# Kernel tuning notes

Measured on AMD Instinct MI355X. Metric: run time of the kernel, lower is better.

## Reference

```python
import jax, jax.numpy as jnp
import numpy as np

B, S, D_IN, D_OUT, H = 2, 2048, 1024, 1024, 16
HD = D_OUT // H  # 64


def setup_inputs() -> dict:
    key = jax.random.key(0)
    ks = jax.random.split(key, 6)
    s = 0.02
    return {
        "x": jax.random.normal(ks[0], (B, S, D_IN), dtype=jnp.float32),
        "W_q": jax.random.normal(ks[1], (D_IN, D_OUT), dtype=jnp.float32) * s,
        "W_k": jax.random.normal(ks[2], (D_IN, D_OUT), dtype=jnp.float32) * s,
        "W_v": jax.random.normal(ks[3], (D_IN, D_OUT), dtype=jnp.float32) * s,
        "W_o": jax.random.normal(ks[4], (D_OUT, D_OUT), dtype=jnp.float32) * s,
        "b_o": jax.random.normal(ks[5], (D_OUT,), dtype=jnp.float32) * s,
    }


def reference(x, W_q, W_k, W_v, W_o, b_o):
    b, n, _ = x.shape
    # project and split heads: [b, h, n, hd]
    q = (x @ W_q).reshape(b, n, H, HD).transpose(0, 2, 1, 3)
    k = (x @ W_k).reshape(b, n, H, HD).transpose(0, 2, 1, 3)
    v = (x @ W_v).reshape(b, n, H, HD).transpose(0, 2, 1, 3)
    scores = jnp.einsum("bhqd,bhkd->bhqk", q, k) / jnp.sqrt(jnp.float32(HD))
    causal = jnp.tril(jnp.ones((n, n), dtype=bool))
    scores = jnp.where(causal, scores, -jnp.inf)
    attn = jax.nn.softmax(scores, axis=-1)  # dropout p=0.0 -> identity
    ctx = jnp.einsum("bhqk,bhkd->bhqd", attn, v)
    ctx = ctx.transpose(0, 2, 1, 3).reshape(b, n, D_OUT)
    return ctx @ W_o + b_o
```

## Files before the change

kernel.cpp:

```cpp
#include <hip/hip_runtime.h>

#define B_    2
#define S_    2048
#define DIN   1024
#define DOUT  1024
#define H_    16
#define HD_   64
#define M_    (B_ * S_)

typedef __bf16 bf16x8 __attribute__((ext_vector_type(8)));
typedef float  f32x4  __attribute__((ext_vector_type(4)));

__device__ __forceinline__ f32x4 MFMA(bf16x8 a, bf16x8 b, f32x4 c) {
    return __builtin_amdgcn_mfma_f32_16x16x32_bf16(a, b, c, 0, 0, 0);
}

__device__ __forceinline__ unsigned short f2b(float f) {
    union { float f; unsigned int u; } v; v.f = f;
    unsigned int u = v.u;
    return (unsigned short)((u + 0x7fffu + ((u >> 16) & 1u)) >> 16);
}

__device__ __forceinline__ unsigned pack2(float a, float b) {
    union { __bf16 h[2]; unsigned u; } cv;
    cv.h[0] = (__bf16)a; cv.h[1] = (__bf16)b;
    return cv.u;
}

#define GLDS(gp, lp) __builtin_amdgcn_global_load_lds( \
    (const __attribute__((address_space(1))) void*)(gp), \
    (__attribute__((address_space(3))) void*)(lp), 16, 0, 0)

#define QSCALE 0.1803368801111204f

__global__ __launch_bounds__(256) void k_cvt_all(const float* __restrict__ x,
                                                 const float* __restrict__ Wq,
                                                 const float* __restrict__ Wk,
                                                 const float* __restrict__ Wv,
                                                 const float* __restrict__ Wo,
                                                 unsigned short* __restrict__ xb,
                                                 unsigned short* __restrict__ WqkvT,
                                                 unsigned short* __restrict__ WoT) {
    __shared__ __align__(16) float tile[64][68];
    int bid = blockIdx.x;
    int tid = threadIdx.x;
    if (bid < 1024) {
#pragma unroll
        for (int j = 0; j < 4; j++) {
            int i = bid * 4096 + j * 1024 + tid * 4;
            float4 v = *reinterpret_cast<const float4*>(x + i);
            ushort4 o;
            o.x = f2b(v.x); o.y = f2b(v.y); o.z = f2b(v.z); o.w = f2b(v.w);
            *reinterpret_cast<ushort4*>(xb + i) = o;
        }
        return;
    }
    int wb = bid - 1024;
    int w = wb >> 8;
    int t = wb & 255;
    const float* src = (w == 0) ? Wq : (w == 1) ? Wk : (w == 2) ? Wv : Wo;
    unsigned short* dst = (w < 3) ? WqkvT + (size_t)w * 1024 * DIN : WoT;
    int k0 = (t >> 4) * 64, n0 = (t & 15) * 64;
#pragma unroll
    for (int j = 0; j < 4; j++) {
        int idx = j * 256 + tid;
        int r = idx >> 4, c4g = idx & 15;
        int sg = c4g ^ ((r >> 3) & 7);
        *reinterpret_cast<float4*>(&tile[r][sg * 4]) =
            *reinterpret_cast<const float4*>(&src[(size_t)(k0 + r) * DOUT + n0 + c4g * 4]);
    }
    __syncthreads();
#pragma unroll
    for (int j = 0; j < 2; j++) {
        int idx = j * 256 + tid;
        int n = idx >> 3, gk = (idx & 7) * 8;
        int g = n >> 2, e = n & 3;
        unsigned short o[8];
#pragma unroll
        for (int u = 0; u < 8; u++) {
            int k = gk + u;
            o[u] = f2b(tile[k][((g ^ ((k >> 3) & 7)) << 2) + e]);
        }
        *reinterpret_cast<int4*>(&dst[(size_t)(n0 + n) * DIN + k0 + gk]) =
            *reinterpret_cast<int4*>(o);
    }
}

template <int OUT_MODE, int BM>
__global__ __launch_bounds__(256) void k_gemm(const unsigned short* __restrict__ A,
                                              const unsigned short* __restrict__ Bt,
                                              unsigned short* __restrict__ Cq,
                                              unsigned short* __restrict__ Ck,
                                              unsigned short* __restrict__ Cvt,
                                              float* __restrict__ Cf,
                                              const float* __restrict__ bias,
                                              int M, int N, int K, int bxg) {
    constexpr int MI  = BM / 32;
    constexpr int ASZ = BM * 32;
    constexpr int BSZ = 128 * 32;
    constexpr int ACH = BM / 64;
    constexpr int STG = 2 * (ASZ + BSZ);
    constexpr int SMEM_N = (OUT_MODE == 0 && STG < 17408) ? 17408 : STG;
    __shared__ __align__(16) unsigned short smem[SMEM_N];

    int bid = blockIdx.x;
    int xcd = bid & 7;
    int r = bid >> 3;
    int byg = (M / BM) >> 2;
    int by = (xcd >> 1) * byg + r / bxg;
    int bx = (xcd & 1) * bxg + r % bxg;
    int m0 = by * BM, n0 = bx * 128;

    int tid = threadIdx.x;
    int wid = tid >> 6, lane = tid & 63;
    int wm = wid >> 1, wn = wid & 1;
    int lr = lane & 15, lg = lane >> 4;

    f32x4 acc[MI][4] = {};

    int srow = lane >> 2;
    int scol = ((lane & 3) ^ (srow & 3)) * 8;
    int runit = (lg ^ (lr & 3)) * 8;

#define STAGE_G(buf, k0)                                                       \
    {                                                                          \
        unsigned short* Ad = smem + (buf) * ASZ;                               \
        unsigned short* Bd = smem + 2 * ASZ + (buf) * BSZ;                     \
        _Pragma("unroll")                                                      \
        for (int c = 0; c < ACH; c++) {                                        \
            int chunk = wid * ACH + c;                                         \
            int row = chunk * 16 + srow;                                       \
            GLDS(A + (size_t)(m0 + row) * K + (k0) + scol,                     \
                 (char*)Ad + chunk * 1024);                                    \
        }                                                                      \
        _Pragma("unroll")                                                      \
        for (int c = 0; c < 2; c++) {                                          \
            int chunk = wid * 2 + c;                                           \
            int row = chunk * 16 + srow;                                       \
            GLDS(Bt + (size_t)(n0 + row) * K + (k0) + scol,                    \
                 (char*)Bd + chunk * 1024);                                    \
        }                                                                      \
    }

    STAGE_G(0, 0)
    __syncthreads();

    int nkt = K >> 5;
    for (int kt = 0; kt < nkt; kt++) {
        int buf = kt & 1;
        if (kt + 1 < nkt) STAGE_G(buf ^ 1, (kt + 1) * 32)

        const unsigned short* Asr = smem + buf * ASZ;
        const unsigned short* Bsr = smem + 2 * ASZ + buf * BSZ;
        bf16x8 af[MI], bf[4];
#pragma unroll
        for (int mi = 0; mi < MI; mi++)
            af[mi] = *reinterpret_cast<const bf16x8*>(
                &Asr[(wm * (BM / 2) + mi * 16 + lr) * 32 + runit]);
#pragma unroll
        for (int ni = 0; ni < 4; ni++)
            bf[ni] = *reinterpret_cast<const bf16x8*>(
                &Bsr[(wn * 64 + ni * 16 + lr) * 32 + runit]);
#pragma unroll
        for (int mi = 0; mi < MI; mi++)
#pragma unroll
            for (int ni = 0; ni < 4; ni++)
                acc[mi][ni] = MFMA(af[mi], bf[ni], acc[mi][ni]);

        asm volatile("s_waitcnt vmcnt(0)" ::: "memory");
        __builtin_amdgcn_s_barrier();
    }

    if (OUT_MODE == 2) {
        for (int mi = 0; mi < MI; mi++)
            for (int ni = 0; ni < 4; ni++)
                for (int i = 0; i < 4; i++) {
                    int row = m0 + wm * (BM / 2) + mi * 16 + lg * 4 + i;
                    int col = n0 + wn * 64 + ni * 16 + lr;
                    Cf[(size_t)row * N + col] = acc[mi][ni][i] + bias[col];
                }
    } else if (n0 < 2048) {
        unsigned short* Cd = (n0 < 1024) ? Cq : Ck;
        int cb = (n0 < 1024) ? 0 : 1024;
        float sc = (n0 < 1024) ? QSCALE : 1.0f;
        for (int mi = 0; mi < MI; mi++)
            for (int ni = 0; ni < 4; ni++)
                for (int i = 0; i < 4; i++) {
                    int row = m0 + wm * (BM / 2) + mi * 16 + lg * 4 + i;
                    int col = n0 + wn * 64 + ni * 16 + lr;
                    Cd[(size_t)row * 1024 + (col - cb)] = f2b(acc[mi][ni][i] * sc);
                }
    } else {
        unsigned short* Lt = smem;
        for (int mi = 0; mi < MI; mi++)
            for (int ni = 0; ni < 4; ni++) {
                int cl = wn * 64 + ni * 16 + lr;
                int rl0 = wm * (BM / 2) + mi * 16 + lg * 4;
                uint2 wd;
                wd.x = pack2(acc[mi][ni][0], acc[mi][ni][1]);
                wd.y = pack2(acc[mi][ni][2], acc[mi][ni][3]);
                *reinterpret_cast<uint2*>(&Lt[cl * 136 + rl0]) = wd;
            }
        __syncthreads();
        int b = m0 >> 11, ms = m0 & (S_ - 1);
        int bh64 = (b * H_ + ((n0 - 2048) >> 6)) * 64;
#pragma unroll
        for (int it = 0; it < 4; it++) {
            int cl = it * 32 + (tid >> 3);
            int ss = (tid & 7) * 16;
            int4 v0 = *reinterpret_cast<int4*>(&Lt[cl * 136 + ss]);
            int4 v1 = *reinterpret_cast<int4*>(&Lt[cl * 136 + ss + 8]);
            unsigned short* dp = Cvt + (size_t)(bh64 + cl) * S_ + ms + ss;
            *reinterpret_cast<int4*>(dp) = v0;
            *reinterpret_cast<int4*>(dp + 8) = v1;
        }
    }
#undef STAGE_G
}

__global__ __launch_bounds__(512, 4) void k_attn(const unsigned short* __restrict__ Q,
                                                 const unsigned short* __restrict__ Kg,
                                                 const unsigned short* __restrict__ Vt,
                                                 unsigned short* __restrict__ ctx) {
    int bid = blockIdx.x;
    int xcd = bid & 7;
    int k   = bid >> 3;
    int p   = k >> 2;
    int bh  = xcd * 4 + (k & 3);
    int b = bh >> 4, h = bh & 15;
    int tid = threadIdx.x, wid = tid >> 6, lane = tid & 63;
    int lr = lane & 15, lg = lane >> 4;
    int qtB = 31 - p;
    int qt = (wid < 4) ? qtB : p;
    int q0 = qt * 64 + (wid & 3) * 16;

    __shared__ __align__(16) unsigned short Ks[4][64 * 64];
    __shared__ __align__(16) unsigned short Vs[4][64 * 64];
    __shared__ __align__(16) unsigned p_lds32[8][16 * 32];
    unsigned* pl32 = p_lds32[wid];

    const unsigned short* Qp = Q  + (size_t)b * S_ * DOUT + (size_t)h * HD_;
    const unsigned short* Kp = Kg + (size_t)b * S_ * DOUT + (size_t)h * HD_;
    const unsigned short* Vp = Vt + (size_t)(b * H_ + h) * HD_ * S_;

    bf16x8 qf0 = *reinterpret_cast<const bf16x8*>(&Qp[(size_t)(q0 + lr) * DOUT + lg * 8]);
    bf16x8 qf1 = *reinterpret_cast<const bf16x8*>(&Qp[(size_t)(q0 + lr) * DOUT + 32 + lg * 8]);
    asm volatile("" : "+v"(qf0), "+v"(qf1));

    int srow = lane >> 3;
    int scol = ((lane & 7) ^ srow) * 8;

#define STAGE_KV(buf, t)                                                           \
    {                                                                              \
        int kv0_ = (t) * 64;                                                       \
        int krow = wid * 8 + srow;                                                 \
        GLDS(Kp + (size_t)(kv0_ + krow) * DOUT + scol,                             \
             (char*)&Ks[buf][0] + wid * 1024);                                     \
        GLDS(Vp + (size_t)krow * S_ + kv0_ + scol,                                 \
             (char*)&Vs[buf][0] + wid * 1024);                                     \
    }

    int ntile = qtB + 1;
    STAGE_KV(0, 0)
    STAGE_KV(1, 1)

    f32x4 o[4] = {};
    float l = 0.f;
    int rxor = (lr & 7) << 4;
    int qg = q0 + lr;

    int cur = 0;
    for (int t = 0; t < ntile; t++) {
        int ahead = ntile - 1 - t;
        if (ahead >= 2) {
            STAGE_KV((cur + 2) & 3, t + 2)
            asm volatile("s_waitcnt vmcnt(4)" ::: "memory");
        } else if (ahead == 1) {
            asm volatile("s_waitcnt vmcnt(2)" ::: "memory");
        } else {
            asm volatile("s_waitcnt vmcnt(0)" ::: "memory");
        }
        __builtin_amdgcn_s_barrier();

        if (t <= qt) {
            const unsigned short* Kt = Ks[cur];
            const unsigned short* Vl = Vs[cur];
            int kv0 = t * 64;

            f32x4 s[4] = {};
            __builtin_amdgcn_s_setprio(1);
#pragma unroll
            for (int nf = 0; nf < 4; nf++)
#pragma unroll
                for (int kk = 0; kk < 2; kk++) {
                    bf16x8 kf = *reinterpret_cast<const bf16x8*>(
                        &Kt[(nf * 16 + lr) * 64 + (((kk * 64 + lg * 16) ^ rxor) >> 1)]);
                    s[nf] = MFMA(kf, kk ? qf1 : qf0, s[nf]);
                }
            __builtin_amdgcn_s_setprio(0);

            if (t == qt) {
#pragma unroll
                for (int nf = 0; nf < 4; nf++)
#pragma unroll
                    for (int i = 0; i < 4; i++)
                        if (kv0 + nf * 16 + lg * 4 + i > qg) s[nf][i] = -2000.0f;
            }

            f32x4 acc = {};
#pragma unroll
            for (int nf = 0; nf < 4; nf++) {
                f32x4 pv;
#pragma unroll
                for (int i = 0; i < 4; i++) pv[i] = exp2f(s[nf][i]);
                acc += pv;
                int unit = (nf * 2 + (lg >> 1)) ^ (lr & 7);
                uint2 wd; wd.x = pack2(pv[0], pv[1]); wd.y = pack2(pv[2], pv[3]);
                *reinterpret_cast<uint2*>(&pl32[lr * 32 + unit * 4 + (lg & 1) * 2]) = wd;
            }
            l += (acc[0] + acc[1]) + (acc[2] + acc[3]);

            bf16x8 pf[2];
#pragma unroll
            for (int kvb = 0; kvb < 2; kvb++)
                pf[kvb] = *reinterpret_cast<const bf16x8*>(
                    &pl32[lr * 32 + (((kvb * 4 + lg) ^ (lr & 7)) * 4)]);

            __builtin_amdgcn_s_setprio(1);
#pragma unroll
            for (int nd = 0; nd < 4; nd++)
#pragma unroll
                for (int kk = 0; kk < 2; kk++) {
                    bf16x8 vf = *reinterpret_cast<const bf16x8*>(
                        &Vl[(nd * 16 + lr) * 64 + (((kk * 64 + lg * 16) ^ rxor) >> 1)]);
                    o[nd] = MFMA(pf[kk], vf, o[nd]);
                }
            __builtin_amdgcn_s_setprio(0);
        }

        cur = (cur + 1) & 3;
    }

    l += __shfl_xor(l, 16, 64);
    l += __shfl_xor(l, 32, 64);

#pragma unroll
    for (int i = 0; i < 4; i++) {
        float li = __shfl(l, lg * 4 + i, 16);
        float r = __builtin_amdgcn_rcpf(li);
#pragma unroll
        for (int nd = 0; nd < 4; nd++)
            ((__bf16*)ctx)[((size_t)b * S_ + q0 + lg * 4 + i) * DOUT + h * HD_ + nd * 16 + lr] =
                (__bf16)(o[nd][i] * r);
    }
#undef STAGE_KV
}

extern "C" void kernel_launch(void* const* d_in, const int* in_sizes, int n_in,
                              void* d_out, int out_size, void* d_ws, size_t ws_size,
                              hipStream_t stream) {
    const float* x  = (const float*)d_in[0];
    const float* Wq = (const float*)d_in[1];
    const float* Wk = (const float*)d_in[2];
    const float* Wv = (const float*)d_in[3];
    const float* Wo = (const float*)d_in[4];
    const float* bo = (const float*)d_in[5];
    float* out = (float*)d_out;
    char* ws = (char*)d_ws;
    const size_t MB = 1u << 20;

    unsigned short* xb    = (unsigned short*)(ws);
    unsigned short* ctx   = (unsigned short*)(ws);
    unsigned short* WqkvT = (unsigned short*)(ws + 8 * MB);
    unsigned short* WoT   = (unsigned short*)(ws + 14 * MB);
    unsigned short* Qb    = (unsigned short*)(ws + 16 * MB);
    unsigned short* Kb    = (unsigned short*)(ws + 24 * MB);
    unsigned short* Vtb   = (unsigned short*)(ws + 32 * MB);

    (void)in_sizes; (void)n_in; (void)out_size; (void)ws_size;

    k_cvt_all<<<2048, 256, 0, stream>>>(x, Wq, Wk, Wv, Wo, xb, WqkvT, WoT);

    k_gemm<0, 128><<<768, 256, 0, stream>>>(xb, WqkvT, Qb, Kb, Vtb, nullptr, nullptr,
                                            M_, 3072, DIN, 12);

    k_attn<<<512, 512, 0, stream>>>(Qb, Kb, Vtb, ctx);

    k_gemm<2, 64><<<512, 256, 0, stream>>>(ctx, WoT, nullptr, nullptr, nullptr,
                                           out, bo, M_, DOUT, DOUT, 4);
}
```

Baseline: 101.0 us.

## Replace double-buffered K32 GEMM pipeline with single-buffer K64 tiles

The projection GEMM now stages 64-wide K tiles into a single shared buffer, using an 8-way XOR swizzle, instead of double-buffering 32-wide tiles. Each tile does two MFMA k-steps between two __syncthreads per iteration. This halves the number of loop iterations and barriers per K and keeps shared memory usage the same, but global loads no longer overlap with MFMA compute, so load latency is exposed every iteration.

```diff
diff --git a/kernel.cpp b/kernel.cpp
--- a/kernel.cpp
+++ b/kernel.cpp
@@ -96,12 +96,14 @@
                                               const float* __restrict__ bias,
                                               int M, int N, int K, int bxg) {
     constexpr int MI  = BM / 32;
-    constexpr int ASZ = BM * 32;
-    constexpr int BSZ = 128 * 32;
-    constexpr int ACH = BM / 64;
-    constexpr int STG = 2 * (ASZ + BSZ);
+    constexpr int ASZ = BM * 64;
+    constexpr int BSZ = 128 * 64;
+    constexpr int ACH = BM / 32;
+    constexpr int STG = ASZ + BSZ;
     constexpr int SMEM_N = (OUT_MODE == 0 && STG < 17408) ? 17408 : STG;
     __shared__ __align__(16) unsigned short smem[SMEM_N];
+    unsigned short* As = smem;
+    unsigned short* Bs = smem + ASZ;
 
     int bid = blockIdx.x;
     int xcd = bid & 7;
@@ -118,57 +120,43 @@
 
     f32x4 acc[MI][4] = {};
 
-    int srow = lane >> 2;
-    int scol = ((lane & 3) ^ (srow & 3)) * 8;
-    int runit = (lg ^ (lr & 3)) * 8;
-
-#define STAGE_G(buf, k0)                                                       \
-    {                                                                          \
-        unsigned short* Ad = smem + (buf) * ASZ;                               \
-        unsigned short* Bd = smem + 2 * ASZ + (buf) * BSZ;                     \
-        _Pragma("unroll")                                                      \
-        for (int c = 0; c < ACH; c++) {                                        \
-            int chunk = wid * ACH + c;                                         \
-            int row = chunk * 16 + srow;                                       \
-            GLDS(A + (size_t)(m0 + row) * K + (k0) + scol,                     \
-                 (char*)Ad + chunk * 1024);                                    \
-        }                                                                      \
-        _Pragma("unroll")                                                      \
-        for (int c = 0; c < 2; c++) {                                          \
-            int chunk = wid * 2 + c;                                           \
-            int row = chunk * 16 + srow;                                       \
-            GLDS(Bt + (size_t)(n0 + row) * K + (k0) + scol,                    \
-                 (char*)Bd + chunk * 1024);                                    \
-        }                                                                      \
-    }
-
-    STAGE_G(0, 0)
-    __syncthreads();
-
-    int nkt = K >> 5;
-    for (int kt = 0; kt < nkt; kt++) {
-        int buf = kt & 1;
-        if (kt + 1 < nkt) STAGE_G(buf ^ 1, (kt + 1) * 32)
-
-        const unsigned short* Asr = smem + buf * ASZ;
-        const unsigned short* Bsr = smem + 2 * ASZ + buf * BSZ;
-        bf16x8 af[MI], bf[4];
-#pragma unroll
-        for (int mi = 0; mi < MI; mi++)
-            af[mi] = *reinterpret_cast<const bf16x8*>(
-                &Asr[(wm * (BM / 2) + mi * 16 + lr) * 32 + runit]);
-#pragma unroll
-        for (int ni = 0; ni < 4; ni++)
-            bf[ni] = *reinterpret_cast<const bf16x8*>(
-                &Bsr[(wn * 64 + ni * 16 + lr) * 32 + runit]);
-#pragma unroll
-        for (int mi = 0; mi < MI; mi++)
+    int srow = lane >> 3;
+    int scol = ((lane & 7) ^ srow) * 8;
+    int rsw  = lr & 7;
+
+    for (int k0 = 0; k0 < K; k0 += 64) {
+#pragma unroll
+        for (int c = 0; c < ACH; c++) {
+            int chunk = wid * ACH + c;
+            int row = chunk * 8 + srow;
+            GLDS(A + (size_t)(m0 + row) * K + k0 + scol, (char*)As + chunk * 1024);
+        }
+#pragma unroll
+        for (int c = 0; c < 4; c++) {
+            int chunk = wid * 4 + c;
+            int row = chunk * 8 + srow;
+            GLDS(Bt + (size_t)(n0 + row) * K + k0 + scol, (char*)Bs + chunk * 1024);
+        }
+        __syncthreads();
+
+#pragma unroll
+        for (int kk = 0; kk < 2; kk++) {
+            bf16x8 af[MI], bf[4];
+#pragma unroll
+            for (int mi = 0; mi < MI; mi++)
+                af[mi] = *reinterpret_cast<const bf16x8*>(
+                    &As[(wm * (BM / 2) + mi * 16 + lr) * 64 + (((kk * 4 + lg) ^ rsw) * 8)]);
 #pragma unroll
             for (int ni = 0; ni < 4; ni++)
-                acc[mi][ni] = MFMA(af[mi], bf[ni], acc[mi][ni]);
-
-        asm volatile("s_waitcnt vmcnt(0)" ::: "memory");
-        __builtin_amdgcn_s_barrier();
+                bf[ni] = *reinterpret_cast<const bf16x8*>(
+                    &Bs[(wn * 64 + ni * 16 + lr) * 64 + (((kk * 4 + lg) ^ rsw) * 8)]);
+#pragma unroll
+            for (int mi = 0; mi < MI; mi++)
+#pragma unroll
+                for (int ni = 0; ni < 4; ni++)
+                    acc[mi][ni] = MFMA(af[mi], bf[ni], acc[mi][ni]);
+        }
+        __syncthreads();
     }
 
     if (OUT_MODE == 2) {
@@ -215,7 +203,6 @@
             *reinterpret_cast<int4*>(dp + 8) = v1;
         }
     }
-#undef STAGE_G
 }
 
 __global__ __launch_bounds__(512, 4) void k_attn(const unsigned short* __restrict__ Q,
```

Result: slower. 108.6 us (+7.5%).
